# Kernel optimization log

Measured on AMD Instinct MI355X. Metric: run time of the kernel, lower is better.

## Reference

```python
import jax, jax.numpy as jnp
import numpy as np

T, W, H = 3072, 2048, 1024   # tokens, words, hidden
C, S = 32, 3                 # labels, score channels (start/end/inside)
HID = 512                    # scorer MLP hidden
MAXW = 12                    # max span width
THR = 0.5                    # extraction threshold
N = W * MAXW                 # fixed number of enumerated spans


def setup_inputs() -> dict:
    key = jax.random.key(0)
    ks = jax.random.split(key, 16)
    hidden_states = jax.random.normal(ks[0], (T, H), jnp.float32) * 0.05
    # each word's first subword carries word_id+1; other tokens carry 0
    first_pos = (jnp.arange(W) * T // W).astype(jnp.int32)
    words_mask = jnp.zeros((T,), jnp.int32).at[first_pos].set(jnp.arange(1, W + 1, dtype=jnp.int32))
    labels_embeds = jax.random.normal(ks[1], (C, H), jnp.float32) * 0.05
    p = lambda k, shp: jax.random.normal(k, shp, jnp.float32) * 0.02
    return dict(
        hidden_states=hidden_states,
        words_mask=words_mask,
        labels_embeds=labels_embeds,
        Wt=p(ks[2], (H, 2 * H)), bt=jnp.zeros((2 * H,), jnp.float32),
        Wl=p(ks[3], (H, 2 * H)), bl=jnp.zeros((2 * H,), jnp.float32),
        W1a=p(ks[4], (H, HID)), W1b=p(ks[5], (H, HID)), W1c=p(ks[6], (H, HID)),
        b1=jnp.zeros((HID,), jnp.float32),
        W2=p(ks[7], (HID, S)), b2=jnp.zeros((S,), jnp.float32),
        Wsp1=p(ks[8], (2 * H, H)), bsp1=jnp.zeros((H,), jnp.float32),
        Wsp2=p(ks[9], (H, H)), bsp2=jnp.zeros((H,), jnp.float32),
    )


def reference(hidden_states, words_mask, labels_embeds,
              Wt, bt, Wl, bl, W1a, W1b, W1c, b1, W2, b2,
              Wsp1, bsp1, Wsp2, bsp2):
    # --- scatter token embeddings into word slots (dummy slot W absorbs mask==0) ---
    idx = jnp.where(words_mask > 0, words_mask - 1, W)
    we = jnp.zeros((W + 1, H), hidden_states.dtype).at[idx].add(hidden_states)[:W]  # [W,H]

    # --- scorer: proj to (2,H) halves, pairwise features, MLP -> [W,C,S] ---
    tok = (we @ Wt + bt).reshape(W, 2, H)
    lab = (labels_embeds @ Wl + bl).reshape(C, 2, H)
    t0, t1 = tok[:, 0], tok[:, 1]
    l0, l1 = lab[:, 0], lab[:, 1]
    # first MLP layer on concat([t0, l0, t1*l1]) computed as split matmuls
    h = (t0 @ W1a)[:, None, :] + (l0 @ W1b)[None, :, :] \
        + jnp.einsum('wh,ch,hd->wcd', t1, l1, W1c)
    h = jax.nn.relu(h + b1)
    scores = h @ W2 + b2  # [W,C,S]

    # --- threshold span extraction (fixed-shape enumeration of widths < MAXW) ---
    probs = jax.nn.sigmoid(scores)
    is_start = jnp.any(probs[..., 0] >= THR, axis=1)  # [W]
    is_end = jnp.any(probs[..., 1] >= THR, axis=1)    # [W]
    starts = jnp.repeat(jnp.arange(W), MAXW)          # [N]
    ends_raw = starts + jnp.tile(jnp.arange(MAXW), W)
    valid = ends_raw < W
    ends = jnp.minimum(ends_raw, W - 1)
    span_mask = valid & is_start[starts] & is_end[ends]  # [N]
    span_idx = jnp.stack([starts, ends], axis=-1)        # [N,2] int

    # --- span_rep_layer: gather start/end word embeds, 2-layer projection ---
    idxm = span_idx * span_mask[:, None].astype(span_idx.dtype)
    sp = jnp.concatenate([we[idxm[:, 0]], we[idxm[:, 1]]], axis=-1)  # [N,2H]
    span_rep = jax.nn.relu(sp @ Wsp1 + bsp1) @ Wsp2 + bsp2           # [N,H]

    # einsum 'BND,BCD->BNC' with B=1
    span_logits = span_rep @ labels_embeds.T  # [N,C]

    # pack_shape_prefixed_tensor equivalent: flat float payload
    flat = jnp.concatenate([
        scores.ravel(),
        span_idx.astype(scores.dtype).ravel(),
        span_mask.astype(scores.dtype),
        span_logits.ravel(),
    ])
    return flat
```

## Files before the change

### kernel.cpp

```cpp
#include <hip/hip_runtime.h>
#include <hip/hip_bf16.h>

#define W_WORDS 2048
#define H_DIM   1024
#define C_LAB   32
#define HID_D   512
#define MAXW    12
#define NSPAN   (W_WORDS * MAXW)

typedef __attribute__((ext_vector_type(8))) short bf16x8;
typedef __attribute__((ext_vector_type(4))) float f32x4;
typedef __attribute__((ext_vector_type(4))) int i32x4;
typedef __attribute__((ext_vector_type(8))) int i32x8;

__device__ __forceinline__ unsigned short f2b(float x) {
  union { float f; unsigned int i; } v; v.f = x;
  unsigned int r = v.i + 0x7FFFu + ((v.i >> 16) & 1u);
  return (unsigned short)(r >> 16);
}
__device__ __forceinline__ float b2f(unsigned short b) {
  union { float f; unsigned int i; } v; v.i = ((unsigned int)b) << 16;
  return v.f;
}

__device__ __forceinline__ unsigned char f2e4m3(float x) {
  union { float f; unsigned u; } v; v.f = x;
  unsigned sign = (v.u >> 31) << 7;
  v.u &= 0x7FFFFFFFu;
  if (v.f > 448.f) v.f = 448.f;
  int e8 = (int)(v.u >> 23) - 120;
  unsigned r;
  if (e8 >= 1) {
    unsigned m = v.u & 0x7FFFFFu;
    unsigned keep = m >> 20;
    unsigned rest = m & 0xFFFFFu;
    keep += (rest > 0x80000u) || (rest == 0x80000u && (keep & 1u));
    if (keep == 8u) { keep = 0u; ++e8; }
    if (e8 >= 16) { e8 = 15; keep = 6u; }
    else if (e8 == 15 && keep == 7u) keep = 6u;
    r = (unsigned)((e8 << 3) | keep);
  } else {
    int m = (int)(v.f * 512.f + 0.5f);
    r = (m >= 8) ? 0x08u : (unsigned)m;
  }
  return (unsigned char)(r | sign);
}

#define GLOAD_LDS16(g, l)                                                    \
  __builtin_amdgcn_global_load_lds(                                          \
      (const __attribute__((address_space(1))) unsigned int*)(g),            \
      (__attribute__((address_space(3))) unsigned int*)(l), 16, 0, 0)

__global__ void mega0_k(const float* __restrict__ hs, const int* __restrict__ wm,
    unsigned short* __restrict__ we_b,
    const float* __restrict__ Wt, const float* __restrict__ W1a,
    const float* __restrict__ Wsp1, const float* __restrict__ W1c,
    const float* __restrict__ Wsp2,
    unsigned short* __restrict__ WtT, unsigned short* __restrict__ W1aT,
    unsigned short* __restrict__ Wsp1Tc, float* __restrict__ W1cT,
    float* __restrict__ Wsp2T, unsigned short* __restrict__ Wtb0) {
  if (blockIdx.z == 6) {
    int t = blockIdx.y * 96 + blockIdx.x;
    int m = wm[t];
    if (m <= 0) return;
    const float* src = hs + (size_t)t * H_DIM;
    unsigned short* dst = we_b + (size_t)(m - 1) * H_DIM;
    int i = (threadIdx.y * 32 + threadIdx.x) * 4;
    float4 v = *(const float4*)(src + i);
    *(ushort4*)(dst + i) = make_ushort4(f2b(v.x), f2b(v.y), f2b(v.z), f2b(v.w));
    return;
  }
  int c0 = blockIdx.x * 32, r0 = blockIdx.y * 32;
  if (blockIdx.z == 7) {
    if (c0 >= 1024) return;
    for (int i = threadIdx.y; i < 32; i += 8)
      Wtb0[(size_t)(r0 + i) * 1024 + c0 + threadIdx.x] =
          f2b(Wt[(size_t)(r0 + i) * 2048 + c0 + threadIdx.x]);
    return;
  }
  const float* in;
  void* out;
  int R, C, obf;
  switch (blockIdx.z) {
    case 0: in = Wt;   out = WtT;    R = 1024; C = 2048; obf = 1; break;
    case 1: in = W1a;  out = W1aT;   R = 1024; C = 512;  obf = 1; break;
    case 2: in = Wsp1; out = Wsp1Tc; R = 1024; C = 1024; obf = 1; break;
    case 3: in = Wsp1 + 1048576; out = Wsp1Tc + 1048576; R = 1024; C = 1024; obf = 1; break;
    case 4: in = W1c;  out = W1cT;   R = 1024; C = 512;  obf = 0; break;
    default: in = Wsp2; out = Wsp2T; R = 1024; C = 1024; obf = 0; break;
  }
  if (c0 >= C || r0 >= R) return;
  __shared__ float tile[32][33];
  for (int i = threadIdx.y; i < 32; i += 8)
    tile[i][threadIdx.x] = in[(size_t)(r0 + i) * C + c0 + threadIdx.x];
  __syncthreads();
  if (obf) {
    unsigned short* o = (unsigned short*)out;
    for (int i = threadIdx.y; i < 32; i += 8)
      o[(size_t)(c0 + i) * R + r0 + threadIdx.x] = f2b(tile[threadIdx.x][i]);
  } else {
    float* o = (float*)out;
    for (int i = threadIdx.y; i < 32; i += 8)
      o[(size_t)(c0 + i) * R + r0 + threadIdx.x] = tile[threadIdx.x][i];
  }
}

__device__ __forceinline__ void rgemm8_body(int N, int M,
    const float* __restrict__ A, int lda, const float* __restrict__ B, int ldb,
    const float* __restrict__ bias, float* __restrict__ out, int ldc,
    int bx, int by, float* shf) {
  float (*Asm)[1024] = (float(*)[1024])shf;
  float (*red)[16][8] = (float(*)[16][8])(shf + 8192);
  int m0 = by * 8;
  for (int idx = threadIdx.x; idx < 8 * 1024; idx += 256) {
    int mm = idx >> 10, kk = idx & 1023;
    Asm[mm][kk] = (m0 + mm < M) ? A[(size_t)(m0 + mm) * lda + kk] : 0.f;
  }
  __syncthreads();
  int tx = threadIdx.x & 15, ty = threadIdx.x >> 4;
  int n = bx * 16 + tx;
  float acc[8] = {0.f, 0.f, 0.f, 0.f, 0.f, 0.f, 0.f, 0.f};
  if (n < N) {
    for (int k = ty * 64; k < ty * 64 + 64; ++k) {
      float bv = B[(size_t)k * ldb + n];
#pragma unroll
      for (int mm = 0; mm < 8; ++mm) acc[mm] = fmaf(Asm[mm][k], bv, acc[mm]);
    }
  }
#pragma unroll
  for (int mm = 0; mm < 8; ++mm) red[ty][tx][mm] = acc[mm];
  __syncthreads();
  if (ty < 8 && n < N && m0 + ty < M) {
    float s = 0.f;
#pragma unroll
    for (int q = 0; q < 16; ++q) s += red[q][tx][ty];
    if (bias) s += bias[n];
    out[(size_t)(m0 + ty) * ldc + n] = s;
  }
}

__global__ __launch_bounds__(256) void rgemm8z_k(
    const float* __restrict__ L, const float* __restrict__ Wl,
    const float* __restrict__ bl, float* __restrict__ lab,
    const float* __restrict__ Wsp2T, float* __restrict__ MmTf) {
  __shared__ float shf[10240];
  if (blockIdx.z == 0) {
    rgemm8_body(2048, 32, L, 1024, Wl, 2048, bl, lab, 2048, blockIdx.x, blockIdx.y, shf);
  } else {
    if (blockIdx.x >= 64) return;
    rgemm8_body(1024, 32, L, 1024, Wsp2T, 1024, nullptr, MmTf, 1024,
                blockIdx.x, blockIdx.y, shf);
  }
}

__global__ __launch_bounds__(256) void mega1_k(
    const float* __restrict__ lab, const float* __restrict__ W1cT,
    unsigned char* __restrict__ KT8,
    const float* __restrict__ W1b, const float* __restrict__ b1,
    float* __restrict__ BvecB,
    const float* __restrict__ bsp2, const float* __restrict__ L,
    float* __restrict__ cv, const float* __restrict__ MmTf,
    unsigned short* __restrict__ MmTb, const float* __restrict__ W2,
    unsigned short* __restrict__ W2padT, const float* __restrict__ bsp1,
    unsigned short* __restrict__ bsp1b,
    const float* __restrict__ bt, const float* __restrict__ W1a,
    float* __restrict__ bt0A) {
  __shared__ float shf[10240];
  int g = blockIdx.x;
  if (g < 8192) {
    size_t gid = (size_t)g * 256 + threadIdx.x;
    int row = (int)(gid >> 7);
    int h0 = ((int)gid & 127) * 8;
    int c = row >> 9, d = row & 511;
    const float* lp = lab + (size_t)c * 2048 + 1024 + h0;
    const float* wp = W1cT + (size_t)d * 1024 + h0;
    float4 l0 = *(const float4*)lp, l1 = *(const float4*)(lp + 4);
    float4 w0 = *(const float4*)wp, w1 = *(const float4*)(wp + 4);
    unsigned u0 = (unsigned)f2e4m3(l0.x * w0.x * 1024.f)
                | ((unsigned)f2e4m3(l0.y * w0.y * 1024.f) << 8)
                | ((unsigned)f2e4m3(l0.z * w0.z * 1024.f) << 16)
                | ((unsigned)f2e4m3(l0.w * w0.w * 1024.f) << 24);
    unsigned u1 = (unsigned)f2e4m3(l1.x * w1.x * 1024.f)
                | ((unsigned)f2e4m3(l1.y * w1.y * 1024.f) << 8)
                | ((unsigned)f2e4m3(l1.z * w1.z * 1024.f) << 16)
                | ((unsigned)f2e4m3(l1.w * w1.w * 1024.f) << 24);
    *(uint2*)(KT8 + (size_t)row * 1024 + h0) = make_uint2(u0, u1);
  } else if (g < 8320) {
    int b = g - 8192;
    rgemm8_body(512, 32, lab, 2048, W1b, 512, b1, BvecB, 512, b & 31, b >> 5, shf);
  } else {
    int b = g - 8320;
    if (b < 32) {
      int c = b;
      float a = 0.f;
      for (int k = threadIdx.x; k < 1024; k += 256)
        a = fmaf(bsp2[k], L[(size_t)c * 1024 + k], a);
#pragma unroll
      for (int off = 32; off; off >>= 1) a += __shfl_down(a, off);
      if ((threadIdx.x & 63) == 0) shf[threadIdx.x >> 6] = a;
      __syncthreads();
      if (threadIdx.x == 0) cv[c] = shf[0] + shf[1] + shf[2] + shf[3];
    } else if (b < 64) {
      int i = (b - 32) * 1024 + threadIdx.x * 4;
      float4 v = *(const float4*)(MmTf + i);
      *(ushort4*)(MmTb + i) = make_ushort4(f2b(v.x), f2b(v.y), f2b(v.z), f2b(v.w));
    } else if (b < 96) {
      int i = (b - 64) * 256 + threadIdx.x;
      int n = i >> 9, d = i & 511;
      W2padT[i] = f2b(n < 3 ? W2[d * 3 + n] : 0.f);
    } else if (b == 96) {
      int i = threadIdx.x * 4;
      float4 v = *(const float4*)(bsp1 + i);
      *(ushort4*)(bsp1b + i) = make_ushort4(f2b(v.x), f2b(v.y), f2b(v.z), f2b(v.w));
    } else {
      float (*red)[16] = (float(*)[16])shf;
      int tx = threadIdx.x & 15, ty = threadIdx.x >> 4;
      int d = (b - 97) * 16 + tx;
      float a = 0.f;
      for (int k = ty * 64; k < ty * 64 + 64; ++k)
        a = fmaf(bt[k], W1a[(size_t)k * 512 + d], a);
      red[ty][tx] = a;
      __syncthreads();
      if (ty == 0) {
        float s = 0.f;
#pragma unroll
        for (int q = 0; q < 16; ++q) s += red[q][tx];
        bt0A[d] = s;
      }
    }
  }
}

template <int MODE>
__global__ __launch_bounds__(256) void gemm_k(
    const unsigned short* __restrict__ A, const unsigned short* __restrict__ BT,
    int N, int K,
    float* __restrict__ outF,
    unsigned short* __restrict__ out0, unsigned char* __restrict__ out8,
    unsigned short* __restrict__ out2,
    const float* __restrict__ bias, const float* __restrict__ bias2) {
  __shared__ __align__(16) unsigned short smem[2][16384];
  int tid = threadIdx.x;
  int lane = tid & 63, wid = tid >> 6;
  int wr = wid >> 1, wc = wid & 1;
  int row0 = blockIdx.y * 128, col0 = blockIdx.x * 128;

  f32x4 zero4 = {0.f, 0.f, 0.f, 0.f};
  f32x4 acc[4][4];
#pragma unroll
  for (int i = 0; i < 4; ++i)
#pragma unroll
    for (int j = 0; j < 4; ++j) acc[i][j] = zero4;

  int srow = tid >> 3;
  int scol = ((tid & 7) ^ (srow & 7)) * 8;
  const unsigned short* gA = A + (size_t)(row0 + srow) * K + scol;
  const unsigned short* gB = BT + (size_t)(col0 + srow) * K + scol;

  int fr = lane & 15, hi = lane >> 4;

#define G_STAGE(buf, kt)                                                     \
  {                                                                          \
    unsigned short* dA = smem[buf] + tid * 8;                                \
    unsigned short* dB = smem[buf] + 8192 + tid * 8;                         \
    _Pragma("unroll")                                                        \
    for (int i2 = 0; i2 < 4; ++i2) {                                         \
      GLOAD_LDS16(gA + (size_t)(i2 * 32) * K + (kt), dA + i2 * 2048);        \
      GLOAD_LDS16(gB + (size_t)(i2 * 32) * K + (kt), dB + i2 * 2048);        \
    }                                                                        \
  }

  G_STAGE(0, 0);

  int nt = K >> 6;
  for (int t = 0; t < nt; ++t) {
    if (t + 1 < nt) {
      G_STAGE((t + 1) & 1, (t + 1) << 6);
      asm volatile("s_waitcnt vmcnt(8)" ::: "memory");
    } else {
      asm volatile("s_waitcnt vmcnt(0)" ::: "memory");
    }
    __builtin_amdgcn_sched_barrier(0);
    __builtin_amdgcn_s_barrier();
    __builtin_amdgcn_sched_barrier(0);

    const unsigned short* As = smem[t & 1];
    const unsigned short* Bs = smem[t & 1] + 8192;
    bf16x8 af[4][2], bfr[4][2];
#pragma unroll
    for (int mi = 0; mi < 4; ++mi) {
      int rl = wr * 64 + mi * 16 + fr;
#pragma unroll
      for (int kk = 0; kk < 2; ++kk)
        af[mi][kk] = *(const bf16x8*)&As[rl * 64 + (((kk << 2) | hi) ^ (rl & 7)) * 8];
    }
#pragma unroll
    for (int ni = 0; ni < 4; ++ni) {
      int rl = wc * 64 + ni * 16 + fr;
#pragma unroll
      for (int kk = 0; kk < 2; ++kk)
        bfr[ni][kk] = *(const bf16x8*)&Bs[rl * 64 + (((kk << 2) | hi) ^ (rl & 7)) * 8];
    }
#pragma unroll
    for (int kk = 0; kk < 2; ++kk)
#pragma unroll
      for (int mi = 0; mi < 4; ++mi)
#pragma unroll
        for (int ni = 0; ni < 4; ++ni)
          acc[mi][ni] = __builtin_amdgcn_mfma_f32_16x16x32_bf16(af[mi][kk], bfr[ni][kk],
                                                                acc[mi][ni], 0, 0, 0);
    __builtin_amdgcn_sched_barrier(0);
    __builtin_amdgcn_s_barrier();
  }
#undef G_STAGE

  int rbase = row0 + wr * 64 + (hi << 2);
  int cbase = col0 + wc * 64 + fr;
#pragma unroll
  for (int mi = 0; mi < 4; ++mi) {
#pragma unroll
    for (int ni = 0; ni < 4; ++ni) {
      int ccol = cbase + ni * 16;
#pragma unroll
      for (int j = 0; j < 4; ++j) {
        int r = rbase + mi * 16 + j;
        float v = acc[mi][ni][j];
        if (MODE == 3) {
          out0[(size_t)r * N + ccol] = f2b(v);
        } else {
          if (ccol < 1024) {
            out8[(size_t)r * 1024 + ccol] = f2e4m3((v + bias[1024 + ccol]) * 16.f);
          } else if (ccol < 3072) {
            out2[(size_t)r * 2048 + (ccol - 1024)] = f2b(v);
          } else {
            outF[(size_t)r * 512 + (ccol - 3072)] = v + bias2[ccol - 3072];
          }
        }
      }
    }
  }
}

__global__ __launch_bounds__(256) void egemm_k(
    const unsigned char* __restrict__ A,
    const unsigned char* __restrict__ BT,
    const float* __restrict__ avec, const float* __restrict__ bvec,
    const unsigned short* __restrict__ w2t, float* __restrict__ sPart) {
  __shared__ __align__(16) unsigned char smem[2][32768];
  int tid = threadIdx.x;
  int lane = tid & 63, wid = tid >> 6;
  int wr = wid >> 1, wc = wid & 1;
  int bid = blockIdx.x;
  int xcd = bid & 7, ii = bid >> 3;
  int sg = ii >> 6, inner = ii & 63;
  int rb = ((sg >> 1) << 3) | (inner & 7);
  int cb = xcd * 16 + (((sg & 1) << 3) | (inner >> 3));
  int row0 = rb * 128, col0 = cb * 128, cbq = cb & 3;

  f32x4 zero4 = {0.f, 0.f, 0.f, 0.f};
  f32x4 acc[4][4];
#pragma unroll
  for (int i = 0; i < 4; ++i)
#pragma unroll
    for (int j = 0; j < 4; ++j) acc[i][j] = zero4;

  int srow = tid >> 3;
  int scolB = ((tid & 7) ^ (srow & 7)) * 16;
  const unsigned char* gA = A + (size_t)(row0 + srow) * 1024 + scolB;
  const unsigned char* gB = BT + (size_t)(col0 + srow) * 1024 + scolB;

  int fr = lane & 15, hi = lane >> 4;

#define E_STAGE(buf, ktB)                                                    \
  {                                                                          \
    unsigned char* dA = smem[buf] + tid * 16;                                \
    unsigned char* dB = smem[buf] + 16384 + tid * 16;                        \
    _Pragma("unroll")                                                        \
    for (int i2 = 0; i2 < 4; ++i2) {                                         \
      GLOAD_LDS16(gA + (size_t)(i2 * 32) * 1024 + (ktB), dA + i2 * 4096);    \
      GLOAD_LDS16(gB + (size_t)(i2 * 32) * 1024 + (ktB), dB + i2 * 4096);    \
    }                                                                        \
  }

  E_STAGE(0, 0);

  for (int t = 0; t < 8; ++t) {
    if (t + 1 < 8) {
      E_STAGE((t + 1) & 1, (t + 1) * 128);
      asm volatile("s_waitcnt vmcnt(8)" ::: "memory");
    } else {
      asm volatile("s_waitcnt vmcnt(0)" ::: "memory");
    }
    __builtin_amdgcn_sched_barrier(0);
    __builtin_amdgcn_s_barrier();
    __builtin_amdgcn_sched_barrier(0);

    const unsigned char* As = smem[t & 1];
    const unsigned char* Bs = smem[t & 1] + 16384;
    i32x8 af[4], bfr[4];
#pragma unroll
    for (int mi = 0; mi < 4; ++mi) {
      int rl = wr * 64 + mi * 16 + fr;
      i32x4 lo = *(const i32x4*)&As[rl * 128 + (((2 * hi) ^ (rl & 7)) * 16)];
      i32x4 h2 = *(const i32x4*)&As[rl * 128 + (((2 * hi + 1) ^ (rl & 7)) * 16)];
      af[mi][0] = lo[0]; af[mi][1] = lo[1]; af[mi][2] = lo[2]; af[mi][3] = lo[3];
      af[mi][4] = h2[0]; af[mi][5] = h2[1]; af[mi][6] = h2[2]; af[mi][7] = h2[3];
    }
#pragma unroll
    for (int ni = 0; ni < 4; ++ni) {
      int rl = wc * 64 + ni * 16 + fr;
      i32x4 lo = *(const i32x4*)&Bs[rl * 128 + (((2 * hi) ^ (rl & 7)) * 16)];
      i32x4 h2 = *(const i32x4*)&Bs[rl * 128 + (((2 * hi + 1) ^ (rl & 7)) * 16)];
      bfr[ni][0] = lo[0]; bfr[ni][1] = lo[1]; bfr[ni][2] = lo[2]; bfr[ni][3] = lo[3];
      bfr[ni][4] = h2[0]; bfr[ni][5] = h2[1]; bfr[ni][6] = h2[2]; bfr[ni][7] = h2[3];
    }
#pragma unroll
    for (int mi = 0; mi < 4; ++mi)
#pragma unroll
      for (int ni = 0; ni < 4; ++ni)
        acc[mi][ni] = __builtin_amdgcn_mfma_scale_f32_16x16x128_f8f6f4(
            af[mi], bfr[ni], acc[mi][ni], 0, 0, 0, 127u, 0, 127u);
    __builtin_amdgcn_sched_barrier(0);
    __builtin_amdgcn_s_barrier();
  }
#undef E_STAGE

  unsigned short* hsm = (unsigned short*)&smem[0][0];
  int cc = col0 >> 9;
  int dg0 = col0 & 511;
  const float inv = 6.103515625e-05f;
#pragma unroll
  for (int mi = 0; mi < 4; ++mi) {
#pragma unroll
    for (int j = 0; j < 4; ++j) {
      int rl = wr * 64 + hi * 4 + mi * 16 + j;
      const float* avp = avec + (size_t)(row0 + rl) * 512 + dg0;
      const float* bvp = bvec + (size_t)cc * 512 + dg0;
#pragma unroll
      for (int ni = 0; ni < 4; ++ni) {
        int cl = wc * 64 + ni * 16 + fr;
        float v = acc[mi][ni][j] * inv + avp[cl] + bvp[cl];
        v = fmaxf(v, 0.f);
        int slot = cl >> 3;
        hsm[rl * 128 + (((slot ^ rl) & 7) << 3) + (slot & 8) * 8 + (cl & 7)] = f2b(v);
      }
    }
  }
  __syncthreads();
  f32x4 s0 = zero4, s1 = zero4;
  int r0l = wid * 32 + fr;
  int r1l = wid * 32 + 16 + fr;
#pragma unroll
  for (int kt2 = 0; kt2 < 4; ++kt2) {
    int slot = kt2 * 4 + hi;
    bf16x8 a0 = *(const bf16x8*)&hsm[r0l * 128 + (((slot ^ r0l) & 7) << 3) + (slot & 8) * 8];
    bf16x8 a1 = *(const bf16x8*)&hsm[r1l * 128 + (((slot ^ r1l) & 7) << 3) + (slot & 8) * 8];
    bf16x8 b = *(const bf16x8*)&w2t[(size_t)fr * 512 + dg0 + kt2 * 32 + hi * 8];
    s0 = __builtin_amdgcn_mfma_f32_16x16x32_bf16(a0, b, s0, 0, 0, 0);
    s1 = __builtin_amdgcn_mfma_f32_16x16x32_bf16(a1, b, s1, 0, 0, 0);
  }
  if (fr < 3) {
    float* sp = sPart + ((size_t)cbq * 2048 + row0) * 96 + cc * 3 + fr;
#pragma unroll
    for (int j = 0; j < 4; ++j) {
      sp[(size_t)(wid * 32 + hi * 4 + j) * 96] = s0[j];
      sp[(size_t)(wid * 32 + 16 + hi * 4 + j) * 96] = s1[j];
    }
  }
}

__global__ __launch_bounds__(256) void foldmask_k(const float* __restrict__ part,
    const float* __restrict__ b2, float* __restrict__ outS,
    int* __restrict__ is_s, int* __restrict__ is_e) {
  __shared__ float sc[192];
  int b = blockIdx.x;
  int i = threadIdx.x;
  if (i < 192) {
    int idx = b * 192 + i;
    float s = b2[i % 3] + part[idx] + part[196608 + idx] +
              part[2 * 196608 + idx] + part[3 * 196608 + idx];
    outS[idx] = s;
    sc[i] = s;
  }
  __syncthreads();
  if (i < 2) {
    int s = 0, e = 0;
#pragma unroll
    for (int c = 0; c < 32; ++c) {
      s |= (sc[i * 96 + c * 3 + 0] >= 0.f);
      e |= (sc[i * 96 + c * 3 + 1] >= 0.f);
    }
    is_s[2 * b + i] = s;
    is_e[2 * b + i] = e;
  }
}

__global__ __launch_bounds__(256) void spanfuse_k(
    const unsigned short* __restrict__ UVb, const unsigned short* __restrict__ bsp1b,
    const unsigned short* __restrict__ MmTb, const float* __restrict__ cvv,
    const int* __restrict__ is_s, const int* __restrict__ is_e,
    float* __restrict__ outIdx, float* __restrict__ outMask,
    float* __restrict__ outLog) {
  __shared__ __align__(16) unsigned short Rs[4][2][16][32];
  int tid = threadIdx.x, lane = tid & 63, w = tid >> 6;
  int fr = lane & 15, hi = lane >> 4;
  int row = lane >> 2, q = lane & 3;
  int n = blockIdx.x * 64 + w * 16 + row;
  int wi = n / MAXW;
  int j = n - wi * MAXW;
  int er = wi + j;
  int valid = er < W_WORDS;
  int e = valid ? er : (W_WORDS - 1);
  int mask = (valid && is_s[wi] && is_e[e]) ? 1 : 0;
  if (q == 0) {
    outIdx[2 * n] = (float)wi;
    outIdx[2 * n + 1] = (float)e;
    outMask[n] = (float)mask;
  }
  int si = mask ? wi : 0, ei = mask ? e : 0;
  const unsigned short* Up = UVb + (size_t)si * 2048 + q * 8;
  const unsigned short* Vp = UVb + (size_t)ei * 2048 + 1024 + q * 8;
  const unsigned short* bp = bsp1b + q * 8;
  const unsigned short* M0 = MmTb + (size_t)fr * 1024 + hi * 8;
  const unsigned short* M1 = MmTb + (size_t)(16 + fr) * 1024 + hi * 8;
  unsigned short* wRs0 = &Rs[w][0][0][0];
  unsigned short* wRs1 = &Rs[w][1][0][0];
  int wslot = (q ^ (row & 3)) * 8;
  int rslot = ((hi ^ (fr & 3)) & 3) * 8;
  f32x4 zero4 = {0.f, 0.f, 0.f, 0.f};
  f32x4 a0 = zero4, a1 = zero4;

  bf16x8 u0 = *(const bf16x8*)Up,        v0 = *(const bf16x8*)Vp;
  bf16x8 b0 = *(const bf16x8*)bp;
  bf16x8 u1 = *(const bf16x8*)(Up + 32), v1 = *(const bf16x8*)(Vp + 32);
  bf16x8 b1v = *(const bf16x8*)(bp + 32);
  bf16x8 f00 = *(const bf16x8*)M0,        f10 = *(const bf16x8*)M1;
  bf16x8 f01 = *(const bf16x8*)(M0 + 32), f11 = *(const bf16x8*)(M1 + 32);

  for (int kt = 0; kt < 32; kt += 2) {
    int ka = ((kt + 2) & 31) * 32, kb = ((kt + 3) & 31) * 32;
    bf16x8 nu0 = *(const bf16x8*)(Up + ka), nv0 = *(const bf16x8*)(Vp + ka);
    bf16x8 nb0 = *(const bf16x8*)(bp + ka);
    bf16x8 nu1 = *(const bf16x8*)(Up + kb), nv1 = *(const bf16x8*)(Vp + kb);
    bf16x8 nb1 = *(const bf16x8*)(bp + kb);
    bf16x8 nf00 = *(const bf16x8*)(M0 + ka), nf10 = *(const bf16x8*)(M1 + ka);
    bf16x8 nf01 = *(const bf16x8*)(M0 + kb), nf11 = *(const bf16x8*)(M1 + kb);

    bf16x8 o0, o1;
#pragma unroll
    for (int i = 0; i < 8; ++i) {
      o0[i] = (short)f2b(fmaxf(b2f((unsigned short)u0[i]) + b2f((unsigned short)v0[i]) +
                               b2f((unsigned short)b0[i]), 0.f));
      o1[i] = (short)f2b(fmaxf(b2f((unsigned short)u1[i]) + b2f((unsigned short)v1[i]) +
                               b2f((unsigned short)b1v[i]), 0.f));
    }
    *(bf16x8*)&wRs0[row * 32 + wslot] = o0;
    *(bf16x8*)&wRs1[row * 32 + wslot] = o1;
    asm volatile("s_waitcnt lgkmcnt(0)" ::: "memory");
    bf16x8 fa0 = *(const bf16x8*)&wRs0[fr * 32 + rslot];
    bf16x8 fa1 = *(const bf16x8*)&wRs1[fr * 32 + rslot];
    a0 = __builtin_amdgcn_mfma_f32_16x16x32_bf16(fa0, f00, a0, 0, 0, 0);
    a1 = __builtin_amdgcn_mfma_f32_16x16x32_bf16(fa0, f10, a1, 0, 0, 0);
    a0 = __builtin_amdgcn_mfma_f32_16x16x32_bf16(fa1, f01, a0, 0, 0, 0);
    a1 = __builtin_amdgcn_mfma_f32_16x16x32_bf16(fa1, f11, a1, 0, 0, 0);
    u0 = nu0; v0 = nv0; b0 = nb0;
    u1 = nu1; v1 = nv1; b1v = nb1;
    f00 = nf00; f10 = nf10; f01 = nf01; f11 = nf11;
  }

  int n0 = blockIdx.x * 64 + w * 16;
  float c0 = cvv[fr], c1 = cvv[16 + fr];
#pragma unroll
  for (int jj = 0; jj < 4; ++jj) {
    int nn = n0 + hi * 4 + jj;
    outLog[(size_t)nn * 32 + fr] = a0[jj] + c0;
    outLog[(size_t)nn * 32 + 16 + fr] = a1[jj] + c1;
  }
}

extern "C" void kernel_launch(void* const* d_in, const int* in_sizes, int n_in,
                              void* d_out, int out_size, void* d_ws, size_t ws_size,
                              hipStream_t stream) {
  const float* hs   = (const float*)d_in[0];
  const int*   wm   = (const int*)d_in[1];
  const float* L    = (const float*)d_in[2];
  const float* Wt   = (const float*)d_in[3];
  const float* bt   = (const float*)d_in[4];
  const float* Wl   = (const float*)d_in[5];
  const float* bl   = (const float*)d_in[6];
  const float* W1a  = (const float*)d_in[7];
  const float* W1b  = (const float*)d_in[8];
  const float* W1c  = (const float*)d_in[9];
  const float* b1   = (const float*)d_in[10];
  const float* W2   = (const float*)d_in[11];
  const float* b2   = (const float*)d_in[12];
  const float* Wsp1 = (const float*)d_in[13];
  const float* bsp1 = (const float*)d_in[14];
  const float* Wsp2 = (const float*)d_in[15];
  const float* bsp2 = (const float*)d_in[16];

  char* p = (char*)d_ws;
  auto alloc = [&p](size_t bytes) {
    char* r = p;
    p += (bytes + 255) & ~(size_t)255;
    return r;
  };
  unsigned short* we_b   = (unsigned short*)alloc((size_t)2048 * 1024 * 2);
  unsigned short* WtT    = (unsigned short*)alloc((size_t)2048 * 1024 * 2);
  unsigned short* Wsp1Tc = (unsigned short*)alloc((size_t)2048 * 1024 * 2);
  unsigned short* WfuseT = (unsigned short*)alloc((size_t)512 * 1024 * 2);
  unsigned char*  t1f8   = (unsigned char*)alloc((size_t)2048 * 1024);
  float*          lab    = (float*)alloc((size_t)32 * 2048 * 4);
  unsigned short* W1aT   = (unsigned short*)alloc((size_t)512 * 1024 * 2);
  unsigned short* Wtb0   = (unsigned short*)alloc((size_t)1024 * 1024 * 2);
  float*          Avec   = (float*)alloc((size_t)2048 * 512 * 4);
  float*          BvecB  = (float*)alloc((size_t)32 * 512 * 4);
  float*          bt0A   = (float*)alloc(512 * 4);
  float*          W1cT   = (float*)alloc((size_t)512 * 1024 * 4);
  unsigned char*  KT8    = (unsigned char*)alloc((size_t)16384 * 1024);
  float*          sPart  = (float*)alloc((size_t)4 * 2048 * 96 * 4);
  int*            is_s   = (int*)alloc(2048 * 4);
  int*            is_e   = (int*)alloc(2048 * 4);
  unsigned short* UVb    = (unsigned short*)alloc((size_t)2048 * 2048 * 2);
  float*          Wsp2T  = (float*)alloc((size_t)1024 * 1024 * 4);
  float*          MmTf   = (float*)alloc((size_t)32 * 1024 * 4);
  unsigned short* MmTb   = (unsigned short*)alloc((size_t)32 * 1024 * 2);
  float*          cv     = (float*)alloc(32 * 4);
  unsigned short* W2padT = (unsigned short*)alloc((size_t)16 * 512 * 2);
  unsigned short* bsp1b  = (unsigned short*)alloc((size_t)1024 * 2);

  float* outS    = (float*)d_out;
  float* outIdx  = outS + (size_t)2048 * 32 * 3;
  float* outMask = outIdx + (size_t)NSPAN * 2;
  float* outLog  = outMask + NSPAN;

  mega0_k<<<dim3(96, 32, 8), dim3(32, 8), 0, stream>>>(
      hs, wm, we_b, Wt, W1a, Wsp1, W1c, Wsp2, WtT, W1aT, Wsp1Tc, W1cT, Wsp2T, Wtb0);

  rgemm8z_k<<<dim3(128, 4, 2), 256, 0, stream>>>(L, Wl, bl, lab, Wsp2T, MmTf);

  mega1_k<<<8449, 256, 0, stream>>>(lab, W1cT, KT8, W1b, b1, BvecB,
                                    bsp2, L, cv, MmTf, MmTb, W2, W2padT, bsp1, bsp1b,
                                    bt, W1a, bt0A);

  gemm_k<3><<<dim3(8, 4), 256, 0, stream>>>(W1aT, Wtb0, 1024, 1024, nullptr, WfuseT,
                                            nullptr, nullptr, nullptr, nullptr);
  gemm_k<1><<<dim3(28, 16), 256, 0, stream>>>(we_b, WtT + (size_t)1024 * 1024, 3584, 1024,
                                              Avec, nullptr, t1f8, UVb, bt, bt0A);
  egemm_k<<<2048, 256, 0, stream>>>(t1f8, KT8, Avec, BvecB, W2padT, sPart);

  foldmask_k<<<1024, 256, 0, stream>>>(sPart, b2, outS, is_s, is_e);

  spanfuse_k<<<384, 256, 0, stream>>>(UVb, bsp1b, MmTb, cv, is_s, is_e,
                                      outIdx, outMask, outLog);
}
```

Before: 192.0 us.

## Quantize word embeddings and projection weights to FP8 for the main fused GEMM

Word embeddings, the second half of Wt and Wsp1 are now stored transposed as scaled e4m3 FP8 instead of bf16. The fused weight product is also emitted as FP8. The large 2048x3584 projection GEMM is rewritten as an FP8 kernel using the scaled 16x16x128 f8f6f4 MFMA, rescaling in the epilogue. This halves operand bytes and uses the higher-throughput FP8 matrix path, with a shared LDS swizzle also adopted by egemm_k. The trade-off is reduced accuracy on these projections, which may push results toward the tolerance limit.

```diff
diff --git a/kernel.cpp b/kernel.cpp
--- a/kernel.cpp
+++ b/kernel.cpp
@@ -52,22 +52,26 @@
       (__attribute__((address_space(3))) unsigned int*)(l), 16, 0, 0)
 
 __global__ void mega0_k(const float* __restrict__ hs, const int* __restrict__ wm,
-    unsigned short* __restrict__ we_b,
+    unsigned char* __restrict__ we8,
     const float* __restrict__ Wt, const float* __restrict__ W1a,
     const float* __restrict__ Wsp1, const float* __restrict__ W1c,
     const float* __restrict__ Wsp2,
-    unsigned short* __restrict__ WtT, unsigned short* __restrict__ W1aT,
-    unsigned short* __restrict__ Wsp1Tc, float* __restrict__ W1cT,
+    unsigned char* __restrict__ WtT8, unsigned short* __restrict__ W1aT,
+    unsigned char* __restrict__ Wsp1Tc8, float* __restrict__ W1cT,
     float* __restrict__ Wsp2T, unsigned short* __restrict__ Wtb0) {
   if (blockIdx.z == 6) {
     int t = blockIdx.y * 96 + blockIdx.x;
     int m = wm[t];
     if (m <= 0) return;
     const float* src = hs + (size_t)t * H_DIM;
-    unsigned short* dst = we_b + (size_t)(m - 1) * H_DIM;
+    unsigned char* dst = we8 + (size_t)(m - 1) * H_DIM;
     int i = (threadIdx.y * 32 + threadIdx.x) * 4;
     float4 v = *(const float4*)(src + i);
-    *(ushort4*)(dst + i) = make_ushort4(f2b(v.x), f2b(v.y), f2b(v.z), f2b(v.w));
+    unsigned u = (unsigned)f2e4m3(v.x * 16.f)
+               | ((unsigned)f2e4m3(v.y * 16.f) << 8)
+               | ((unsigned)f2e4m3(v.z * 16.f) << 16)
+               | ((unsigned)f2e4m3(v.w * 16.f) << 24);
+    *(unsigned*)(dst + i) = u;
     return;
   }
   int c0 = blockIdx.x * 32, r0 = blockIdx.y * 32;
@@ -80,21 +84,25 @@
   }
   const float* in;
   void* out;
-  int R, C, obf;
+  int R, C, ld, mode;
   switch (blockIdx.z) {
-    case 0: in = Wt;   out = WtT;    R = 1024; C = 2048; obf = 1; break;
-    case 1: in = W1a;  out = W1aT;   R = 1024; C = 512;  obf = 1; break;
-    case 2: in = Wsp1; out = Wsp1Tc; R = 1024; C = 1024; obf = 1; break;
-    case 3: in = Wsp1 + 1048576; out = Wsp1Tc + 1048576; R = 1024; C = 1024; obf = 1; break;
-    case 4: in = W1c;  out = W1cT;   R = 1024; C = 512;  obf = 0; break;
-    default: in = Wsp2; out = Wsp2T; R = 1024; C = 1024; obf = 0; break;
+    case 0: in = Wt + 1024; out = WtT8; R = 1024; C = 1024; ld = 2048; mode = 2; break;
+    case 1: in = W1a;  out = W1aT;   R = 1024; C = 512;  ld = 512;  mode = 1; break;
+    case 2: in = Wsp1; out = Wsp1Tc8; R = 1024; C = 1024; ld = 1024; mode = 2; break;
+    case 3: in = Wsp1 + 1048576; out = Wsp1Tc8 + 1048576; R = 1024; C = 1024; ld = 1024; mode = 2; break;
+    case 4: in = W1c;  out = W1cT;   R = 1024; C = 512;  ld = 512;  mode = 0; break;
+    default: in = Wsp2; out = Wsp2T; R = 1024; C = 1024; ld = 1024; mode = 0; break;
   }
   if (c0 >= C || r0 >= R) return;
   __shared__ float tile[32][33];
   for (int i = threadIdx.y; i < 32; i += 8)
-    tile[i][threadIdx.x] = in[(size_t)(r0 + i) * C + c0 + threadIdx.x];
+    tile[i][threadIdx.x] = in[(size_t)(r0 + i) * ld + c0 + threadIdx.x];
   __syncthreads();
-  if (obf) {
+  if (mode == 2) {
+    unsigned char* o = (unsigned char*)out;
+    for (int i = threadIdx.y; i < 32; i += 8)
+      o[(size_t)(c0 + i) * R + r0 + threadIdx.x] = f2e4m3(tile[threadIdx.x][i] * 64.f);
+  } else if (mode == 1) {
     unsigned short* o = (unsigned short*)out;
     for (int i = threadIdx.y; i < 32; i += 8)
       o[(size_t)(c0 + i) * R + r0 + threadIdx.x] = f2b(tile[threadIdx.x][i]);
@@ -231,51 +239,39 @@
   }
 }
 
-template <int MODE>
-__global__ __launch_bounds__(256) void gemm_k(
+__global__ __launch_bounds__(256) void wfuse_k(
     const unsigned short* __restrict__ A, const unsigned short* __restrict__ BT,
-    int N, int K,
-    float* __restrict__ outF,
-    unsigned short* __restrict__ out0, unsigned char* __restrict__ out8,
-    unsigned short* __restrict__ out2,
-    const float* __restrict__ bias, const float* __restrict__ bias2) {
+    unsigned char* __restrict__ out8) {
   __shared__ __align__(16) unsigned short smem[2][16384];
   int tid = threadIdx.x;
   int lane = tid & 63, wid = tid >> 6;
   int wr = wid >> 1, wc = wid & 1;
   int row0 = blockIdx.y * 128, col0 = blockIdx.x * 128;
-
   f32x4 zero4 = {0.f, 0.f, 0.f, 0.f};
   f32x4 acc[4][4];
 #pragma unroll
   for (int i = 0; i < 4; ++i)
 #pragma unroll
     for (int j = 0; j < 4; ++j) acc[i][j] = zero4;
-
   int srow = tid >> 3;
   int scol = ((tid & 7) ^ (srow & 7)) * 8;
-  const unsigned short* gA = A + (size_t)(row0 + srow) * K + scol;
-  const unsigned short* gB = BT + (size_t)(col0 + srow) * K + scol;
-
+  const unsigned short* gA = A + (size_t)(row0 + srow) * 1024 + scol;
+  const unsigned short* gB = BT + (size_t)(col0 + srow) * 1024 + scol;
   int fr = lane & 15, hi = lane >> 4;
-
-#define G_STAGE(buf, kt)                                                     \
+#define W_STAGE(buf, kt)                                                     \
   {                                                                          \
     unsigned short* dA = smem[buf] + tid * 8;                                \
     unsigned short* dB = smem[buf] + 8192 + tid * 8;                         \
     _Pragma("unroll")                                                        \
     for (int i2 = 0; i2 < 4; ++i2) {                                         \
-      GLOAD_LDS16(gA + (size_t)(i2 * 32) * K + (kt), dA + i2 * 2048);        \
-      GLOAD_LDS16(gB + (size_t)(i2 * 32) * K + (kt), dB + i2 * 2048);        \
+      GLOAD_LDS16(gA + (size_t)(i2 * 32) * 1024 + (kt), dA + i2 * 2048);     \
+      GLOAD_LDS16(gB + (size_t)(i2 * 32) * 1024 + (kt), dB + i2 * 2048);     \
     }                                                                        \
   }
-
-  G_STAGE(0, 0);
-
-  int nt = K >> 6;
-  for (int t = 0; t < nt; ++t) {
-    if (t + 1 < nt) {
-      G_STAGE((t + 1) & 1, (t + 1) << 6);
+  W_STAGE(0, 0);
+  for (int t = 0; t < 16; ++t) {
+    if (t + 1 < 16) {
+      W_STAGE((t + 1) & 1, (t + 1) << 6);
       asm volatile("s_waitcnt vmcnt(8)" ::: "memory");
     } else {
       asm volatile("s_waitcnt vmcnt(0)" ::: "memory");
@@ -283,7 +279,6 @@
     __builtin_amdgcn_sched_barrier(0);
     __builtin_amdgcn_s_barrier();
     __builtin_amdgcn_sched_barrier(0);
-
     const unsigned short* As = smem[t & 1];
     const unsigned short* Bs = smem[t & 1] + 8192;
     bf16x8 af[4][2], bfr[4][2];
@@ -312,33 +307,115 @@
     __builtin_amdgcn_sched_barrier(0);
     __builtin_amdgcn_s_barrier();
   }
-#undef G_STAGE
-
+#undef W_STAGE
   int rbase = row0 + wr * 64 + (hi << 2);
   int cbase = col0 + wc * 64 + fr;
 #pragma unroll
-  for (int mi = 0; mi < 4; ++mi) {
+  for (int mi = 0; mi < 4; ++mi)
 #pragma unroll
     for (int ni = 0; ni < 4; ++ni) {
       int ccol = cbase + ni * 16;
 #pragma unroll
       for (int j = 0; j < 4; ++j) {
         int r = rbase + mi * 16 + j;
-        float v = acc[mi][ni][j];
-        if (MODE == 3) {
-          out0[(size_t)r * N + ccol] = f2b(v);
+        out8[(size_t)r * 1024 + ccol] = f2e4m3(acc[mi][ni][j] * 64.f);
+      }
+    }
+}
+
+__global__ __launch_bounds__(256) void fgemm_k(
+    const unsigned char* __restrict__ A, const unsigned char* __restrict__ BT,
+    float* __restrict__ Avec, unsigned char* __restrict__ t1f8,
+    unsigned short* __restrict__ UVb,
+    const float* __restrict__ bt, const float* __restrict__ bt0A) {
+  __shared__ __align__(16) unsigned char smem[2][32768];
+  int tid = threadIdx.x;
+  int lane = tid & 63, wid = tid >> 6;
+  int wr = wid >> 1, wc = wid & 1;
+  int row0 = blockIdx.y * 128, col0 = blockIdx.x * 128;
+  f32x4 zero4 = {0.f, 0.f, 0.f, 0.f};
+  f32x4 acc[4][4];
+#pragma unroll
+  for (int i = 0; i < 4; ++i)
+#pragma unroll
+    for (int j = 0; j < 4; ++j) acc[i][j] = zero4;
+  int srow = tid >> 3;
+  int s2 = (tid & 7) ^ (srow & 7);
+  int scolB = (((s2 << 1) | (s2 >> 2)) & 7) * 16;
+  const unsigned char* gA = A + (size_t)(row0 + srow) * 1024 + scolB;
+  const unsigned char* gB = BT + (size_t)(col0 + srow) * 1024 + scolB;
+  int fr = lane & 15, hi = lane >> 4;
+#define F_STAGE(buf, ktB)                                                    \
+  {                                                                          \
+    unsigned char* dA = smem[buf] + tid * 16;                                \
+    unsigned char* dB = smem[buf] + 16384 + tid * 16;                        \
+    _Pragma("unroll")                                                        \
+    for (int i2 = 0; i2 < 4; ++i2) {                                         \
+      GLOAD_LDS16(gA + (size_t)(i2 * 32) * 1024 + (ktB), dA + i2 * 4096);    \
+      GLOAD_LDS16(gB + (size_t)(i2 * 32) * 1024 + (ktB), dB + i2 * 4096);    \
+    }                                                                        \
+  }
+  F_STAGE(0, 0);
+  for (int t = 0; t < 8; ++t) {
+    if (t + 1 < 8) {
+      F_STAGE((t + 1) & 1, (t + 1) * 128);
+      asm volatile("s_waitcnt vmcnt(8)" ::: "memory");
+    } else {
+      asm volatile("s_waitcnt vmcnt(0)" ::: "memory");
+    }
+    __builtin_amdgcn_sched_barrier(0);
+    __builtin_amdgcn_s_barrier();
+    __builtin_amdgcn_sched_barrier(0);
+    const unsigned char* As = smem[t & 1];
+    const unsigned char* Bs = smem[t & 1] + 16384;
+    i32x8 af[4], bfr[4];
+#pragma unroll
+    for (int mi = 0; mi < 4; ++mi) {
+      int rl = wr * 64 + mi * 16 + fr;
+      i32x4 lo = *(const i32x4*)&As[rl * 128 + ((hi ^ (rl & 7)) * 16)];
+      i32x4 h2 = *(const i32x4*)&As[rl * 128 + (((4 + hi) ^ (rl & 7)) * 16)];
+      af[mi][0] = lo[0]; af[mi][1] = lo[1]; af[mi][2] = lo[2]; af[mi][3] = lo[3];
+      af[mi][4] = h2[0]; af[mi][5] = h2[1]; af[mi][6] = h2[2]; af[mi][7] = h2[3];
+    }
+#pragma unroll
+    for (int ni = 0; ni < 4; ++ni) {
+      int rl = wc * 64 + ni * 16 + fr;
+      i32x4 lo = *(const i32x4*)&Bs[rl * 128 + ((hi ^ (rl & 7)) * 16)];
+      i32x4 h2 = *(const i32x4*)&Bs[rl * 128 + (((4 + hi) ^ (rl & 7)) * 16)];
+      bfr[ni][0] = lo[0]; bfr[ni][1] = lo[1]; bfr[ni][2] = lo[2]; bfr[ni][3] = lo[3];
+      bfr[ni][4] = h2[0]; bfr[ni][5] = h2[1]; bfr[ni][6] = h2[2]; bfr[ni][7] = h2[3];
+    }
+#pragma unroll
+    for (int mi = 0; mi < 4; ++mi)
+#pragma unroll
+      for (int ni = 0; ni < 4; ++ni)
+        acc[mi][ni] = __builtin_amdgcn_mfma_scale_f32_16x16x128_f8f6f4(
+            af[mi], bfr[ni], acc[mi][ni], 0, 0, 0, 127u, 0, 127u);
+    __builtin_amdgcn_sched_barrier(0);
+    __builtin_amdgcn_s_barrier();
+  }
+#undef F_STAGE
+  const float inv = 0.0009765625f;
+  int rbase = row0 + wr * 64 + (hi << 2);
+  int cbase = col0 + wc * 64 + fr;
+#pragma unroll
+  for (int mi = 0; mi < 4; ++mi)
+#pragma unroll
+    for (int ni = 0; ni < 4; ++ni) {
+      int ccol = cbase + ni * 16;
+#pragma unroll
+      for (int j = 0; j < 4; ++j) {
+        int r = rbase + mi * 16 + j;
+        float v = acc[mi][ni][j] * inv;
+        if (ccol < 1024) {
+          t1f8[(size_t)r * 1024 + ccol] = f2e4m3((v + bt[1024 + ccol]) * 16.f);
+        } else if (ccol < 3072) {
+          UVb[(size_t)r * 2048 + (ccol - 1024)] = f2b(v);
         } else {
-          if (ccol < 1024) {
-            out8[(size_t)r * 1024 + ccol] = f2e4m3((v + bias[1024 + ccol]) * 16.f);
-          } else if (ccol < 3072) {
-            out2[(size_t)r * 2048 + (ccol - 1024)] = f2b(v);
-          } else {
-            outF[(size_t)r * 512 + (ccol - 3072)] = v + bias2[ccol - 3072];
-          }
+          Avec[(size_t)r * 512 + (ccol - 3072)] = v + bt0A[ccol - 3072];
         }
       }
     }
-  }
 }
 
 __global__ __launch_bounds__(256) void egemm_k(
@@ -365,7 +442,8 @@
     for (int j = 0; j < 4; ++j) acc[i][j] = zero4;
 
   int srow = tid >> 3;
-  int scolB = ((tid & 7) ^ (srow & 7)) * 16;
+  int s2 = (tid & 7) ^ (srow & 7);
+  int scolB = (((s2 << 1) | (s2 >> 2)) & 7) * 16;
   const unsigned char* gA = A + (size_t)(row0 + srow) * 1024 + scolB;
   const unsigned char* gB = BT + (size_t)(col0 + srow) * 1024 + scolB;
 
@@ -401,16 +479,16 @@
 #pragma unroll
     for (int mi = 0; mi < 4; ++mi) {
       int rl = wr * 64 + mi * 16 + fr;
-      i32x4 lo = *(const i32x4*)&As[rl * 128 + (((2 * hi) ^ (rl & 7)) * 16)];
-      i32x4 h2 = *(const i32x4*)&As[rl * 128 + (((2 * hi + 1) ^ (rl & 7)) * 16)];
+      i32x4 lo = *(const i32x4*)&As[rl * 128 + ((hi ^ (rl & 7)) * 16)];
+      i32x4 h2 = *(const i32x4*)&As[rl * 128 + (((4 + hi) ^ (rl & 7)) * 16)];
       af[mi][0] = lo[0]; af[mi][1] = lo[1]; af[mi][2] = lo[2]; af[mi][3] = lo[3];
       af[mi][4] = h2[0]; af[mi][5] = h2[1]; af[mi][6] = h2[2]; af[mi][7] = h2[3];
     }
 #pragma unroll
     for (int ni = 0; ni < 4; ++ni) {
       int rl = wc * 64 + ni * 16 + fr;
-      i32x4 lo = *(const i32x4*)&Bs[rl * 128 + (((2 * hi) ^ (rl & 7)) * 16)];
-      i32x4 h2 = *(const i32x4*)&Bs[rl * 128 + (((2 * hi + 1) ^ (rl & 7)) * 16)];
+      i32x4 lo = *(const i32x4*)&Bs[rl * 128 + ((hi ^ (rl & 7)) * 16)];
+      i32x4 h2 = *(const i32x4*)&Bs[rl * 128 + (((4 + hi) ^ (rl & 7)) * 16)];
       bfr[ni][0] = lo[0]; bfr[ni][1] = lo[1]; bfr[ni][2] = lo[2]; bfr[ni][3] = lo[3];
       bfr[ni][4] = h2[0]; bfr[ni][5] = h2[1]; bfr[ni][6] = h2[2]; bfr[ni][7] = h2[3];
     }
@@ -605,10 +683,10 @@
     p += (bytes + 255) & ~(size_t)255;
     return r;
   };
-  unsigned short* we_b   = (unsigned short*)alloc((size_t)2048 * 1024 * 2);
-  unsigned short* WtT    = (unsigned short*)alloc((size_t)2048 * 1024 * 2);
-  unsigned short* Wsp1Tc = (unsigned short*)alloc((size_t)2048 * 1024 * 2);
-  unsigned short* WfuseT = (unsigned short*)alloc((size_t)512 * 1024 * 2);
+  unsigned char*  we8    = (unsigned char*)alloc((size_t)2048 * 1024);
+  unsigned char*  WtT8    = (unsigned char*)alloc((size_t)1024 * 1024);
+  unsigned char*  Wsp1Tc8 = (unsigned char*)alloc((size_t)2048 * 1024);
+  unsigned char*  WfuseT8 = (unsigned char*)alloc((size_t)512 * 1024);
   unsigned char*  t1f8   = (unsigned char*)alloc((size_t)2048 * 1024);
   float*          lab    = (float*)alloc((size_t)32 * 2048 * 4);
   unsigned short* W1aT   = (unsigned short*)alloc((size_t)512 * 1024 * 2);
@@ -635,7 +713,7 @@
   float* outLog  = outMask + NSPAN;
 
   mega0_k<<<dim3(96, 32, 8), dim3(32, 8), 0, stream>>>(
-      hs, wm, we_b, Wt, W1a, Wsp1, W1c, Wsp2, WtT, W1aT, Wsp1Tc, W1cT, Wsp2T, Wtb0);
+      hs, wm, we8, Wt, W1a, Wsp1, W1c, Wsp2, WtT8, W1aT, Wsp1Tc8, W1cT, Wsp2T, Wtb0);
 
   rgemm8z_k<<<dim3(128, 4, 2), 256, 0, stream>>>(L, Wl, bl, lab, Wsp2T, MmTf);
 
@@ -643,10 +721,10 @@
                                     bsp2, L, cv, MmTf, MmTb, W2, W2padT, bsp1, bsp1b,
                                     bt, W1a, bt0A);
 
-  gemm_k<3><<<dim3(8, 4), 256, 0, stream>>>(W1aT, Wtb0, 1024, 1024, nullptr, WfuseT,
-                                            nullptr, nullptr, nullptr, nullptr);
-  gemm_k<1><<<dim3(28, 16), 256, 0, stream>>>(we_b, WtT + (size_t)1024 * 1024, 3584, 1024,
-                                              Avec, nullptr, t1f8, UVb, bt, bt0A);
+  wfuse_k<<<dim3(8, 4), 256, 0, stream>>>(W1aT, Wtb0, WfuseT8);
+
+  fgemm_k<<<dim3(28, 16), 256, 0, stream>>>(we8, WtT8, Avec, t1f8, UVb, bt, bt0A);
+
   egemm_k<<<2048, 256, 0, stream>>>(t1f8, KT8, Avec, BvecB, W2padT, sPart);
 
   foldmask_k<<<1024, 256, 0, stream>>>(sPart, b2, outS, is_s, is_e);
```

New measurement: 191.7 us. Within noise of the previous version (-0.1%).
